# Kernel tuning notes

Hardware: AMD Instinct MI355X
Metric: run time of the kernel (lower is better)

Reference implementation:

```python
import jax, jax.numpy as jnp
import numpy as np


def rmsnorm(x, w):
    eps = jnp.finfo(x.dtype).eps  # torch nn.RMSNorm default eps=None -> finfo eps
    return x * jax.lax.rsqrt(jnp.mean(x * x, axis=-1, keepdims=True) + eps) * w


def rotary_freqs(n, d, dtype):
    inv_freq = 1.0 / (10000.0 ** (np.arange(0, d, 2, dtype=np.float32) / d))
    t = np.arange(n, dtype=np.float32)
    f = np.einsum('i,j->ij', t, inv_freq)
    f = np.concatenate([f, f], axis=-1)  # (n, d)
    return jnp.asarray(f, dtype=dtype)


def rotate_half(x):
    x1, x2 = jnp.split(x, 2, axis=-1)
    return jnp.concatenate([-x2, x1], axis=-1)


def local_window_attention(q, k, v, w):
    # q,k,v: (b,h,n,d); causal sliding window, exact window: key j allowed iff 0 <= i-j <= w
    b, h, n, d = q.shape
    nw = n // w
    scale = d ** -0.5
    qw = (q * scale).reshape(b, h, nw, w, d)
    kw = k.reshape(b, h, nw, w, d)
    vw = v.reshape(b, h, nw, w, d)
    shift_prev = lambda t: jnp.concatenate([jnp.zeros_like(t[:, :, :1]), t[:, :, :-1]], axis=2)
    kcat = jnp.concatenate([shift_prev(kw), kw], axis=3)  # (b,h,nw,2w,d)
    vcat = jnp.concatenate([shift_prev(vw), vw], axis=3)
    sim = jnp.einsum('bhnid,bhnjd->bhnij', qw, kcat)  # (b,h,nw,w,2w)
    i_pos = jnp.arange(w)[:, None]
    j_rel = jnp.arange(2 * w)[None, :] - w  # relative key position within window pair
    rel = i_pos - j_rel
    allowed = (rel >= 0) & (rel <= w)  # causal + exact window size
    win_idx = jnp.arange(nw)[:, None, None]
    abs_j_ok = (win_idx * w + j_rel[None]) >= 0  # mask zero-padded keys of first window
    mask = allowed[None] & abs_j_ok  # (nw, w, 2w)
    neg = -jnp.finfo(sim.dtype).max
    sim = jnp.where(mask[None, None], sim, neg)
    attn = jax.nn.softmax(sim, axis=-1)
    out = jnp.einsum('bhnij,bhnjd->bhnid', attn, vcat)
    return out.reshape(b, h, n, d)


def setup_inputs() -> dict:
    key = jax.random.key(0)
    k1, k2, k3 = jax.random.split(key, 3)
    b, n, dim, heads, dim_head, window = 4, 8192, 1024, 16, 64, 64
    dim_inner = heads * dim_head
    x = jax.random.normal(k1, (b, n, dim), dtype=jnp.float32)
    w_norm = jnp.ones((dim,), dtype=jnp.float32)
    w_qkv = jax.random.normal(k2, (dim, 3 * dim_inner), dtype=jnp.float32) * 0.02
    w_o = jax.random.normal(k3, (dim_inner, dim), dtype=jnp.float32) * 0.02
    return {"x": x, "w_norm": w_norm, "w_qkv": w_qkv, "w_o": w_o, "heads": heads, "window_size": window}


def reference(x, w_norm, w_qkv, w_o, heads, window_size):
    b, n, dim = x.shape
    xn = rmsnorm(x, w_norm)
    qkv = xn @ w_qkv  # (b,n,3*h*d)
    q, k, v = jnp.split(qkv, 3, axis=-1)
    split = lambda t: t.reshape(b, n, heads, -1).transpose(0, 2, 1, 3)  # b h n d
    q, k, v = split(q), split(k), split(v)
    d = q.shape[-1]
    freqs = rotary_freqs(n, d, q.dtype)  # (n,d)
    cos, sin = jnp.cos(freqs), jnp.sin(freqs)
    rope = lambda t: t * cos + rotate_half(t) * sin
    q, k = rope(q), rope(k)
    out = local_window_attention(q, k, v, window_size)
    out = out.transpose(0, 2, 1, 3).reshape(b, n, -1)  # merge heads
    return out @ w_o
```

## Files before the change

### kernel.cpp

```cpp
#include <hip/hip_runtime.h>
#include <stdint.h>
#include <math.h>

typedef __attribute__((ext_vector_type(4))) float  f32x4;
typedef __attribute__((ext_vector_type(8))) short  bf16x8;
typedef __attribute__((ext_vector_type(4))) short  s16x4;

#define AS1 __attribute__((address_space(1)))
#define AS3 __attribute__((address_space(3)))

static __device__ __forceinline__ void async_ld16(void* lds, const void* g) {
  __builtin_amdgcn_global_load_lds((const AS1 uint32_t*)g, (AS3 uint32_t*)lds, 16, 0, 0);
}

static __device__ __forceinline__ float bf2f(short u) {
  union { uint32_t i; float f; } v; v.i = ((uint32_t)(uint16_t)u) << 16; return v.f;
}
static __device__ __forceinline__ short f2bf(float f) {
  union { float f; uint32_t i; } v; v.f = f;
  uint32_t x = v.i;
  return (short)((x + 0x7fffu + ((x >> 16) & 1u)) >> 16);
}

__global__ __launch_bounds__(256) void k_trig(float* __restrict__ ct, float* __restrict__ st) {
  int idx = blockIdx.x * 256 + threadIdx.x;
  int pos = idx >> 5, i = idx & 31;
  double invf = 1.0 / pow(10000.0, (double)(2 * i) / 64.0);
  float f = (float)((double)pos * invf);
  ct[idx] = cosf(f);
  st[idx] = sinf(f);
}

__global__ __launch_bounds__(256) void k_transpose_cvt(const float* __restrict__ in,
                                                       short* __restrict__ out, int K, int N) {
  __shared__ float tile[64][65];
  int n0 = blockIdx.x * 64, k0 = blockIdx.y * 64;
  int tid = threadIdx.x;
  #pragma unroll
  for (int it = 0; it < 16; ++it) {
    int idx = tid + it * 256;
    int r = idx >> 6, c = idx & 63;
    tile[r][c] = in[(size_t)(k0 + r) * N + (n0 + c)];
  }
  __syncthreads();
  #pragma unroll
  for (int it = 0; it < 16; ++it) {
    int idx = tid + it * 256;
    int r = idx >> 6, c = idx & 63;
    out[(size_t)(n0 + r) * K + (k0 + c)] = f2bf(tile[c][r]);
  }
}

__global__ __launch_bounds__(256) void k_rmsnorm(const float* __restrict__ x,
                                                 const float* __restrict__ w,
                                                 short* __restrict__ xn) {
  int row = blockIdx.x;
  const float* xr = x + (size_t)row * 1024;
  int tid = threadIdx.x;
  f32x4 v = *(const f32x4*)(xr + (tid << 2));
  float ss = v[0]*v[0] + v[1]*v[1] + v[2]*v[2] + v[3]*v[3];
  #pragma unroll
  for (int off = 1; off < 64; off <<= 1) ss += __shfl_xor(ss, off);
  __shared__ float red[4];
  if ((tid & 63) == 0) red[tid >> 6] = ss;
  __syncthreads();
  float tot = red[0] + red[1] + red[2] + red[3];
  float inv = rsqrtf(tot * (1.0f / 1024.0f) + 1.1920928955078125e-07f);
  f32x4 wv = *(const f32x4*)(w + (tid << 2));
  s16x4 o;
  #pragma unroll
  for (int e = 0; e < 4; ++e) o[e] = f2bf(v[e] * inv * wv[e]);
  *(s16x4*)(xn + (size_t)row * 1024 + (tid << 2)) = o;
}

template<bool OUT_BF16>
__global__ __launch_bounds__(256) void k_gemm(const short* __restrict__ A,
                                              const short* __restrict__ Bt,
                                              void* __restrict__ Cout,
                                              int M, int N, int K) {
  __shared__ short As[128 * 32];
  __shared__ short Bs[128 * 32];
  const int tid = threadIdx.x;
  const int wave = tid >> 6, lane = tid & 63;
  const int g = lane >> 4, r = lane & 15;

  const int nwg = gridDim.x, bid = blockIdx.x;
  const int cpx = nwg >> 3;
  const int swz = (bid & 7) * cpx + (bid >> 3);
  const int nbx = N >> 7;
  const int bx = swz % nbx, by = swz / nbx;
  const int m0 = by << 7, n0 = bx << 7;
  const int wr = wave >> 1, wc = wave & 1;

  f32x4 acc[4][4];
  #pragma unroll
  for (int i = 0; i < 4; ++i)
    #pragma unroll
    for (int j = 0; j < 4; ++j)
      #pragma unroll
      for (int e = 0; e < 4; ++e) acc[i][j][e] = 0.0f;

  const int ci0 = wave * 128 + lane, ci1 = ci0 + 64;
  const int ar0 = ci0 >> 2, as0 = (ci0 & 3) ^ ((ar0 >> 1) & 3);
  const int ar1 = ci1 >> 2, as1 = (ci1 & 3) ^ ((ar1 >> 1) & 3);
  const short* Ag0 = A  + (size_t)(m0 + ar0) * K + as0 * 8;
  const short* Ag1 = A  + (size_t)(m0 + ar1) * K + as1 * 8;
  const short* Bg0 = Bt + (size_t)(n0 + ar0) * K + as0 * 8;
  const short* Bg1 = Bt + (size_t)(n0 + ar1) * K + as1 * 8;
  short* Al0 = &As[(wave * 128 + 0)  * 8];
  short* Al1 = &As[(wave * 128 + 64) * 8];
  short* Bl0 = &Bs[(wave * 128 + 0)  * 8];
  short* Bl1 = &Bs[(wave * 128 + 64) * 8];

  for (int k0 = 0; k0 < K; k0 += 32) {
    async_ld16(Al0, Ag0 + k0);
    async_ld16(Al1, Ag1 + k0);
    async_ld16(Bl0, Bg0 + k0);
    async_ld16(Bl1, Bg1 + k0);
    __syncthreads();
    bf16x8 af[4], bfr[4];
    #pragma unroll
    for (int m = 0; m < 4; ++m) {
      int row = wr * 64 + m * 16 + r;
      af[m] = *(const bf16x8*)&As[row * 32 + ((g ^ ((row >> 1) & 3)) * 8)];
    }
    #pragma unroll
    for (int n = 0; n < 4; ++n) {
      int row = wc * 64 + n * 16 + r;
      bfr[n] = *(const bf16x8*)&Bs[row * 32 + ((g ^ ((row >> 1) & 3)) * 8)];
    }
    #pragma unroll
    for (int m = 0; m < 4; ++m)
      #pragma unroll
      for (int n = 0; n < 4; ++n)
        acc[m][n] = __builtin_amdgcn_mfma_f32_16x16x32_bf16(af[m], bfr[n], acc[m][n], 0, 0, 0);
    __syncthreads();
  }

  if (OUT_BF16) {
    short* C = (short*)Cout;
    #pragma unroll
    for (int m = 0; m < 4; ++m) {
      int rowb = m0 + wr * 64 + m * 16 + g * 4;
      #pragma unroll
      for (int n = 0; n < 4; ++n) {
        int col = n0 + wc * 64 + n * 16 + r;
        #pragma unroll
        for (int q = 0; q < 4; ++q) C[(size_t)(rowb + q) * N + col] = f2bf(acc[m][n][q]);
      }
    }
  } else {
    float* C = (float*)Cout;
    #pragma unroll
    for (int m = 0; m < 4; ++m) {
      int rowb = m0 + wr * 64 + m * 16 + g * 4;
      #pragma unroll
      for (int n = 0; n < 4; ++n) {
        int col = n0 + wc * 64 + n * 16 + r;
        #pragma unroll
        for (int q = 0; q < 4; ++q) C[(size_t)(rowb + q) * N + col] = acc[m][n][q];
      }
    }
  }
}

__global__ __launch_bounds__(256) void k_rope(short* __restrict__ qkv,
                                              const float* __restrict__ ct,
                                              const float* __restrict__ st) {
  int t = blockIdx.x * 256 + threadIdx.x;
  int row = t >> 7, rem = t & 127;
  int hp = rem >> 2, d0 = (rem & 3) * 8;
  int part = hp >> 4, h = hp & 15;
  size_t base = (size_t)row * 3072 + part * 1024 + h * 64;
  int pos = row & 8191;
  bf16x8 lo = *(const bf16x8*)(qkv + base + d0);
  bf16x8 hi = *(const bf16x8*)(qkv + base + d0 + 32);
  f32x4 c0 = *(const f32x4*)(ct + pos * 32 + d0);
  f32x4 c1 = *(const f32x4*)(ct + pos * 32 + d0 + 4);
  f32x4 s0 = *(const f32x4*)(st + pos * 32 + d0);
  f32x4 s1 = *(const f32x4*)(st + pos * 32 + d0 + 4);
  bf16x8 olo, ohi;
  #pragma unroll
  for (int e = 0; e < 8; ++e) {
    float c = (e < 4) ? c0[e & 3] : c1[e & 3];
    float s = (e < 4) ? s0[e & 3] : s1[e & 3];
    float xl = bf2f(lo[e]), xh = bf2f(hi[e]);
    olo[e] = f2bf(xl * c - xh * s);
    ohi[e] = f2bf(xh * c + xl * s);
  }
  *(bf16x8*)(qkv + base + d0) = olo;
  *(bf16x8*)(qkv + base + d0 + 32) = ohi;
}

__global__ __launch_bounds__(256) void k_attn(const short* __restrict__ qkv,
                                              short* __restrict__ aout) {
  const int win = blockIdx.x, h = blockIdx.y, bb = blockIdx.z;
  __shared__ short Qs[64 * 64];
  __shared__ short Ks[128 * 64];
  __shared__ short Vt[64 * 128];
  __shared__ short Ps[64 * 128];

  const int tid = threadIdx.x;
  const int wave = tid >> 6, lane = tid & 63;
  const int g = lane >> 4, r = lane & 15;
  const size_t bbase = (size_t)bb * 8192;

  #pragma unroll
  for (int t = 0; t < 2; ++t) {
    int i = wave * 128 + t * 64 + lane;
    int row = i >> 3, seg = i & 7;
    int sseg = seg ^ (row & 7);
    const short* gp = qkv + (bbase + win * 64 + row) * 3072 + h * 64 + sseg * 8;
    async_ld16(&Qs[(wave * 128 + t * 64) * 8], gp);
  }
  #pragma unroll
  for (int t = 0; t < 4; ++t) {
    int i = wave * 256 + t * 64 + lane;
    int row = i >> 3, seg = i & 7;
    int sseg = seg ^ (row & 7);
    int kpos = win * 64 - 64 + row; if (kpos < 0) kpos = 0;
    const short* gp = qkv + (bbase + kpos) * 3072 + 1024 + h * 64 + sseg * 8;
    async_ld16(&Ks[(wave * 256 + t * 64) * 8], gp);
  }
  #pragma unroll
  for (int t = 0; t < 4; ++t) {
    int task = tid + t * 256;
    int j = task >> 3, dseg = task & 7;
    int kpos = win * 64 - 64 + j; if (kpos < 0) kpos = 0;
    bf16x8 v = *(const bf16x8*)(qkv + (bbase + kpos) * 3072 + 2048 + h * 64 + dseg * 8);
    #pragma unroll
    for (int e = 0; e < 8; ++e) {
      int d = dseg * 8 + e;
      Vt[d * 128 + (((j >> 3) ^ (d & 15)) * 8) + (j & 7)] = v[e];
    }
  }
  __syncthreads();

  f32x4 sac[8];
  #pragma unroll
  for (int n = 0; n < 8; ++n)
    #pragma unroll
    for (int e = 0; e < 4; ++e) sac[n][e] = 0.0f;
  {
    bf16x8 aq[2];
    #pragma unroll
    for (int ks = 0; ks < 2; ++ks) {
      int row = wave * 16 + r;
      aq[ks] = *(const bf16x8*)&Qs[row * 64 + (((ks * 4 + g) ^ (row & 7)) * 8)];
    }
    #pragma unroll
    for (int n = 0; n < 8; ++n)
      #pragma unroll
      for (int ks = 0; ks < 2; ++ks) {
        int key = n * 16 + r;
        bf16x8 bk = *(const bf16x8*)&Ks[key * 64 + (((ks * 4 + g) ^ (key & 7)) * 8)];
        sac[n] = __builtin_amdgcn_mfma_f32_16x16x32_bf16(aq[ks], bk, sac[n], 0, 0, 0);
      }
  }

  float pm[8][4], mx[4], sm[4];
  #pragma unroll
  for (int q = 0; q < 4; ++q) mx[q] = -3.0e38f;
  #pragma unroll
  for (int n = 0; n < 8; ++n)
    #pragma unroll
    for (int q = 0; q < 4; ++q) {
      int iq = wave * 16 + g * 4 + q;
      int j = n * 16 + r;
      bool ok = (j >= iq) && (j <= iq + 64) && (win > 0 || j >= 64);
      float s = ok ? sac[n][q] * 0.125f : -3.0e38f;
      pm[n][q] = s;
      mx[q] = fmaxf(mx[q], s);
    }
  #pragma unroll
  for (int q = 0; q < 4; ++q)
    #pragma unroll
    for (int off = 1; off < 16; off <<= 1) mx[q] = fmaxf(mx[q], __shfl_xor(mx[q], off));
  #pragma unroll
  for (int q = 0; q < 4; ++q) sm[q] = 0.0f;
  #pragma unroll
  for (int n = 0; n < 8; ++n)
    #pragma unroll
    for (int q = 0; q < 4; ++q) {
      float p = __expf(pm[n][q] - mx[q]);
      pm[n][q] = p;
      sm[q] += p;
    }
  #pragma unroll
  for (int q = 0; q < 4; ++q) {
    #pragma unroll
    for (int off = 1; off < 16; off <<= 1) sm[q] += __shfl_xor(sm[q], off);
    sm[q] = 1.0f / sm[q];
  }
  #pragma unroll
  for (int n = 0; n < 8; ++n)
    #pragma unroll
    for (int q = 0; q < 4; ++q) {
      int iq = wave * 16 + g * 4 + q;
      int j = n * 16 + r;
      Ps[iq * 128 + (((j >> 3) ^ (iq & 15)) * 8) + (j & 7)] = f2bf(pm[n][q] * sm[q]);
    }
  __syncthreads();

  f32x4 oac[4];
  #pragma unroll
  for (int n = 0; n < 4; ++n)
    #pragma unroll
    for (int e = 0; e < 4; ++e) oac[n][e] = 0.0f;
  #pragma unroll
  for (int ks = 0; ks < 4; ++ks) {
    int rowp = wave * 16 + r;
    bf16x8 ap = *(const bf16x8*)&Ps[rowp * 128 + (((ks * 4 + g) ^ (rowp & 15)) * 8)];
    #pragma unroll
    for (int n = 0; n < 4; ++n) {
      int d = n * 16 + r;
      bf16x8 bv = *(const bf16x8*)&Vt[d * 128 + (((ks * 4 + g) ^ (d & 15)) * 8)];
      oac[n] = __builtin_amdgcn_mfma_f32_16x16x32_bf16(ap, bv, oac[n], 0, 0, 0);
    }
  }
  #pragma unroll
  for (int n = 0; n < 4; ++n)
    #pragma unroll
    for (int q = 0; q < 4; ++q) {
      int iq = wave * 16 + g * 4 + q;
      int d = n * 16 + r;
      int pos = win * 64 + iq;
      aout[(bbase + pos) * 1024 + h * 64 + d] = f2bf(oac[n][q]);
    }
}

extern "C" void kernel_launch(void* const* d_in, const int* in_sizes, int n_in,
                              void* d_out, int out_size, void* d_ws, size_t ws_size,
                              hipStream_t stream) {
  const float* x      = (const float*)d_in[0];
  const float* w_norm = (const float*)d_in[1];
  const float* w_qkv  = (const float*)d_in[2];
  const float* w_o    = (const float*)d_in[3];
  float* out = (float*)d_out;
  (void)in_sizes; (void)n_in; (void)out_size; (void)ws_size;

  const int R = 4 * 8192;

  char* ws = (char*)d_ws;
  size_t off = 0;
  auto alloc = [&](size_t bytes) { char* p = ws + off; off += (bytes + 255) & ~(size_t)255; return p; };
  short* xn   = (short*)alloc((size_t)R * 1024 * 2);
  short* wqT  = (short*)alloc((size_t)3072 * 1024 * 2);
  short* woT  = (short*)alloc((size_t)1024 * 1024 * 2);
  short* qkv  = (short*)alloc((size_t)R * 3072 * 2);
  short* aout = (short*)alloc((size_t)R * 1024 * 2);
  float* ct   = (float*)alloc((size_t)8192 * 32 * 4);
  float* st   = (float*)alloc((size_t)8192 * 32 * 4);

  k_trig<<<1024, 256, 0, stream>>>(ct, st);
  k_transpose_cvt<<<dim3(3072 / 64, 1024 / 64), 256, 0, stream>>>(w_qkv, wqT, 1024, 3072);
  k_transpose_cvt<<<dim3(1024 / 64, 1024 / 64), 256, 0, stream>>>(w_o, woT, 1024, 1024);
  k_rmsnorm<<<R, 256, 0, stream>>>(x, w_norm, xn);
  k_gemm<true><<<(R / 128) * (3072 / 128), 256, 0, stream>>>(xn, wqT, qkv, R, 3072, 1024);
  k_rope<<<16384, 256, 0, stream>>>(qkv, ct, st);
  k_attn<<<dim3(128, 16, 4), 256, 0, stream>>>(qkv, aout);
  k_gemm<false><<<(R / 128) * (1024 / 128), 256, 0, stream>>>(aout, woT, out, R, 1024, 1024);
}
```

Before: 759.3 us.

## Replace GEMMs with 256x256 double-buffered pipelined kernel and fuse RoPE into epilogue

Replaces the 128x128 single-buffered GEMM with a 256x256-tile, 512-thread kernel. It double-buffers 64-wide K slices in LDS, interleaves async global-to-LDS loads with quarter-tile MFMA phases under explicit barriers and waitcnts, and raises wave priority around the MFMA blocks. The rotary embedding is applied to the fp32 accumulators in the QKV GEMM epilogue for the Q and K columns, which removes the separate rope pass over the qkv buffer. The larger tile uses 128KB of LDS and more registers per block, and fewer workgroups are launched for the smaller output GEMM.

```diff
diff --git a/kernel.cpp b/kernel.cpp
--- a/kernel.cpp
+++ b/kernel.cpp
@@ -21,6 +21,12 @@
   uint32_t x = v.i;
   return (short)((x + 0x7fffu + ((x >> 16) & 1u)) >> 16);
 }
+
+#define BAR()   __builtin_amdgcn_s_barrier()
+#define LGKM0() do { asm volatile("s_waitcnt lgkmcnt(0)" ::: "memory"); \
+                     __builtin_amdgcn_sched_barrier(0); } while (0)
+#define VMW4()  asm volatile("s_waitcnt vmcnt(4)" ::: "memory")
+#define PRIO(p) __builtin_amdgcn_s_setprio(p)
 
 __global__ __launch_bounds__(256) void k_trig(float* __restrict__ ct, float* __restrict__ st) {
   int idx = blockIdx.x * 256 + threadIdx.x;
@@ -73,123 +79,163 @@
   *(s16x4*)(xn + (size_t)row * 1024 + (tid << 2)) = o;
 }
 
-template<bool OUT_BF16>
-__global__ __launch_bounds__(256) void k_gemm(const short* __restrict__ A,
-                                              const short* __restrict__ Bt,
-                                              void* __restrict__ Cout,
-                                              int M, int N, int K) {
-  __shared__ short As[128 * 32];
-  __shared__ short Bs[128 * 32];
-  const int tid = threadIdx.x;
+#define STAGE(mi, P, rb, h, kt, buf) do {                                          \
+    const int lrb = (h) * 128 + wrow;                                              \
+    const short* _s0 = (P) + (size_t)((rb) + lrb + srow) * K + (kt) * 64 + xseg * 8;      \
+    const short* _s1 = (P) + (size_t)((rb) + lrb + 8 + srow) * K + (kt) * 64 + xseg * 8;  \
+    async_ld16(&lds[buf][mi][lrb * 64], _s0);                                      \
+    async_ld16(&lds[buf][mi][(lrb + 8) * 64], _s1);                                \
+  } while (0)
+
+#define RDA(buf, mh, m, kk) \
+  (*(const bf16x8*)&lds[buf][0][(wr * 128 + (mh) * 64 + (m) * 16 + r) * 64 + ((((kk) * 4 + g) ^ rs) * 8)])
+#define RDB(buf, nh, n, kk) \
+  (*(const bf16x8*)&lds[buf][1][(wc * 64 + (nh) * 32 + (n) * 16 + r) * 64 + ((((kk) * 4 + g) ^ rs) * 8)])
+
+template<bool OUT_BF16, bool ROPE>
+__global__ __launch_bounds__(512, 2) void k_gemm2(const short* __restrict__ A,
+                                                  const short* __restrict__ Bt,
+                                                  void* __restrict__ Cout,
+                                                  const float* __restrict__ ct,
+                                                  const float* __restrict__ st,
+                                                  int M, int N, int K) {
+  __shared__ short lds[2][2][256 * 64];
+  (void)M;
+  const int tid  = threadIdx.x;
   const int wave = tid >> 6, lane = tid & 63;
   const int g = lane >> 4, r = lane & 15;
+  const int wr = wave >> 2, wc = wave & 3;
+  const int rs = r & 7;
 
   const int nwg = gridDim.x, bid = blockIdx.x;
   const int cpx = nwg >> 3;
   const int swz = (bid & 7) * cpx + (bid >> 3);
-  const int nbx = N >> 7;
+  const int nbx = N >> 8;
   const int bx = swz % nbx, by = swz / nbx;
-  const int m0 = by << 7, n0 = bx << 7;
-  const int wr = wave >> 1, wc = wave & 1;
-
-  f32x4 acc[4][4];
-  #pragma unroll
-  for (int i = 0; i < 4; ++i)
+  const int m0 = by << 8, n0 = bx << 8;
+  const int NT = K >> 6;
+
+  const int srow = lane >> 3;
+  const int xseg = (lane & 7) ^ srow;
+  const int wrow = wave * 16;
+
+  f32x4 acc[8][4];
+  #pragma unroll
+  for (int i = 0; i < 8; ++i)
     #pragma unroll
     for (int j = 0; j < 4; ++j)
-      #pragma unroll
-      for (int e = 0; e < 4; ++e) acc[i][j][e] = 0.0f;
-
-  const int ci0 = wave * 128 + lane, ci1 = ci0 + 64;
-  const int ar0 = ci0 >> 2, as0 = (ci0 & 3) ^ ((ar0 >> 1) & 3);
-  const int ar1 = ci1 >> 2, as1 = (ci1 & 3) ^ ((ar1 >> 1) & 3);
-  const short* Ag0 = A  + (size_t)(m0 + ar0) * K + as0 * 8;
-  const short* Ag1 = A  + (size_t)(m0 + ar1) * K + as1 * 8;
-  const short* Bg0 = Bt + (size_t)(n0 + ar0) * K + as0 * 8;
-  const short* Bg1 = Bt + (size_t)(n0 + ar1) * K + as1 * 8;
-  short* Al0 = &As[(wave * 128 + 0)  * 8];
-  short* Al1 = &As[(wave * 128 + 64) * 8];
-  short* Bl0 = &Bs[(wave * 128 + 0)  * 8];
-  short* Bl1 = &Bs[(wave * 128 + 64) * 8];
-
-  for (int k0 = 0; k0 < K; k0 += 32) {
-    async_ld16(Al0, Ag0 + k0);
-    async_ld16(Al1, Ag1 + k0);
-    async_ld16(Bl0, Bg0 + k0);
-    async_ld16(Bl1, Bg1 + k0);
-    __syncthreads();
-    bf16x8 af[4], bfr[4];
-    #pragma unroll
-    for (int m = 0; m < 4; ++m) {
-      int row = wr * 64 + m * 16 + r;
-      af[m] = *(const bf16x8*)&As[row * 32 + ((g ^ ((row >> 1) & 3)) * 8)];
-    }
-    #pragma unroll
-    for (int n = 0; n < 4; ++n) {
-      int row = wc * 64 + n * 16 + r;
-      bfr[n] = *(const bf16x8*)&Bs[row * 32 + ((g ^ ((row >> 1) & 3)) * 8)];
-    }
+      acc[i][j] = (f32x4){0.f, 0.f, 0.f, 0.f};
+
+  STAGE(0, A,  m0, 0, 0, 0);
+  STAGE(0, A,  m0, 1, 0, 0);
+  STAGE(1, Bt, n0, 0, 0, 0);
+  STAGE(1, Bt, n0, 1, 0, 0);
+  STAGE(1, Bt, n0, 0, 1, 1);
+  STAGE(0, A,  m0, 0, 1, 1);
+  VMW4(); BAR();
+
+  bf16x8 a[4][2], b0[2][2], b1[2][2];
+  for (int t = 0; t < NT; ++t) {
+    const int cur = t & 1, nxt = cur ^ 1;
+    const int t1 = (t + 1 < NT) ? t + 1 : 0;
+    const int t2 = (t + 2 < NT) ? t + 2 : t + 2 - NT;
+
+    #pragma unroll
+    for (int m = 0; m < 4; ++m) { a[m][0] = RDA(cur, 0, m, 0); a[m][1] = RDA(cur, 0, m, 1); }
+    #pragma unroll
+    for (int n = 0; n < 2; ++n) { b0[n][0] = RDB(cur, 0, n, 0); b0[n][1] = RDB(cur, 0, n, 1); }
+    STAGE(0, A, m0, 1, t1, nxt);
+    BAR(); LGKM0(); PRIO(1);
     #pragma unroll
     for (int m = 0; m < 4; ++m)
       #pragma unroll
-      for (int n = 0; n < 4; ++n)
-        acc[m][n] = __builtin_amdgcn_mfma_f32_16x16x32_bf16(af[m], bfr[n], acc[m][n], 0, 0, 0);
-    __syncthreads();
+      for (int n = 0; n < 2; ++n)
+        #pragma unroll
+        for (int kk = 0; kk < 2; ++kk)
+          acc[m][n] = __builtin_amdgcn_mfma_f32_16x16x32_bf16(a[m][kk], b0[n][kk], acc[m][n], 0, 0, 0);
+    PRIO(0); BAR();
+
+    #pragma unroll
+    for (int n = 0; n < 2; ++n) { b1[n][0] = RDB(cur, 1, n, 0); b1[n][1] = RDB(cur, 1, n, 1); }
+    STAGE(1, Bt, n0, 1, t1, nxt);
+    BAR(); LGKM0(); PRIO(1);
+    #pragma unroll
+    for (int m = 0; m < 4; ++m)
+      #pragma unroll
+      for (int n = 0; n < 2; ++n)
+        #pragma unroll
+        for (int kk = 0; kk < 2; ++kk)
+          acc[m][2 + n] = __builtin_amdgcn_mfma_f32_16x16x32_bf16(a[m][kk], b1[n][kk], acc[m][2 + n], 0, 0, 0);
+    PRIO(0); BAR();
+
+    #pragma unroll
+    for (int m = 0; m < 4; ++m) { a[m][0] = RDA(cur, 1, m, 0); a[m][1] = RDA(cur, 1, m, 1); }
+    STAGE(1, Bt, n0, 0, t2, cur);
+    BAR(); LGKM0(); PRIO(1);
+    #pragma unroll
+    for (int m = 0; m < 4; ++m)
+      #pragma unroll
+      for (int n = 0; n < 2; ++n)
+        #pragma unroll
+        for (int kk = 0; kk < 2; ++kk)
+          acc[4 + m][2 + n] = __builtin_amdgcn_mfma_f32_16x16x32_bf16(a[m][kk], b1[n][kk], acc[4 + m][2 + n], 0, 0, 0);
+    PRIO(0); BAR();
+
+    STAGE(0, A, m0, 0, t2, cur);
+    PRIO(1);
+    #pragma unroll
+    for (int m = 0; m < 4; ++m)
+      #pragma unroll
+      for (int n = 0; n < 2; ++n)
+        #pragma unroll
+        for (int kk = 0; kk < 2; ++kk)
+          acc[4 + m][n] = __builtin_amdgcn_mfma_f32_16x16x32_bf16(a[m][kk], b0[n][kk], acc[4 + m][n], 0, 0, 0);
+    PRIO(0);
+    VMW4(); BAR();
   }
 
   if (OUT_BF16) {
     short* C = (short*)Cout;
-    #pragma unroll
-    for (int m = 0; m < 4; ++m) {
-      int rowb = m0 + wr * 64 + m * 16 + g * 4;
-      #pragma unroll
-      for (int n = 0; n < 4; ++n) {
-        int col = n0 + wc * 64 + n * 16 + r;
-        #pragma unroll
-        for (int q = 0; q < 4; ++q) C[(size_t)(rowb + q) * N + col] = f2bf(acc[m][n][q]);
+    const bool doRope = ROPE && (n0 < 2048);
+    #pragma unroll
+    for (int mi = 0; mi < 8; ++mi) {
+      const int rowb = m0 + wr * 128 + mi * 16 + g * 4;
+      if (doRope) {
+        #pragma unroll
+        for (int q = 0; q < 4; ++q) {
+          const int pos = (rowb + q) & 8191;
+          #pragma unroll
+          for (int ni = 0; ni < 2; ++ni) {
+            const float c = ct[pos * 32 + ni * 16 + r];
+            const float s = st[pos * 32 + ni * 16 + r];
+            const float p0 = acc[mi][ni][q], p1 = acc[mi][ni + 2][q];
+            acc[mi][ni][q]     = p0 * c - p1 * s;
+            acc[mi][ni + 2][q] = p1 * c + p0 * s;
+          }
+        }
+      }
+      #pragma unroll
+      for (int ni = 0; ni < 4; ++ni) {
+        const int col = n0 + wc * 64 + ni * 16 + r;
+        #pragma unroll
+        for (int q = 0; q < 4; ++q)
+          C[(size_t)(rowb + q) * N + col] = f2bf(acc[mi][ni][q]);
       }
     }
   } else {
     float* C = (float*)Cout;
     #pragma unroll
-    for (int m = 0; m < 4; ++m) {
-      int rowb = m0 + wr * 64 + m * 16 + g * 4;
-      #pragma unroll
-      for (int n = 0; n < 4; ++n) {
-        int col = n0 + wc * 64 + n * 16 + r;
-        #pragma unroll
-        for (int q = 0; q < 4; ++q) C[(size_t)(rowb + q) * N + col] = acc[m][n][q];
+    for (int mi = 0; mi < 8; ++mi) {
+      const int rowb = m0 + wr * 128 + mi * 16 + g * 4;
+      #pragma unroll
+      for (int ni = 0; ni < 4; ++ni) {
+        const int col = n0 + wc * 64 + ni * 16 + r;
+        #pragma unroll
+        for (int q = 0; q < 4; ++q)
+          C[(size_t)(rowb + q) * N + col] = acc[mi][ni][q];
       }
     }
   }
-}
-
-__global__ __launch_bounds__(256) void k_rope(short* __restrict__ qkv,
-                                              const float* __restrict__ ct,
-                                              const float* __restrict__ st) {
-  int t = blockIdx.x * 256 + threadIdx.x;
-  int row = t >> 7, rem = t & 127;
-  int hp = rem >> 2, d0 = (rem & 3) * 8;
-  int part = hp >> 4, h = hp & 15;
-  size_t base = (size_t)row * 3072 + part * 1024 + h * 64;
-  int pos = row & 8191;
-  bf16x8 lo = *(const bf16x8*)(qkv + base + d0);
-  bf16x8 hi = *(const bf16x8*)(qkv + base + d0 + 32);
-  f32x4 c0 = *(const f32x4*)(ct + pos * 32 + d0);
-  f32x4 c1 = *(const f32x4*)(ct + pos * 32 + d0 + 4);
-  f32x4 s0 = *(const f32x4*)(st + pos * 32 + d0);
-  f32x4 s1 = *(const f32x4*)(st + pos * 32 + d0 + 4);
-  bf16x8 olo, ohi;
-  #pragma unroll
-  for (int e = 0; e < 8; ++e) {
-    float c = (e < 4) ? c0[e & 3] : c1[e & 3];
-    float s = (e < 4) ? s0[e & 3] : s1[e & 3];
-    float xl = bf2f(lo[e]), xh = bf2f(hi[e]);
-    olo[e] = f2bf(xl * c - xh * s);
-    ohi[e] = f2bf(xh * c + xl * s);
-  }
-  *(bf16x8*)(qkv + base + d0) = olo;
-  *(bf16x8*)(qkv + base + d0 + 32) = ohi;
 }
 
 __global__ __launch_bounds__(256) void k_attn(const short* __restrict__ qkv,
@@ -356,8 +402,7 @@
   k_transpose_cvt<<<dim3(3072 / 64, 1024 / 64), 256, 0, stream>>>(w_qkv, wqT, 1024, 3072);
   k_transpose_cvt<<<dim3(1024 / 64, 1024 / 64), 256, 0, stream>>>(w_o, woT, 1024, 1024);
   k_rmsnorm<<<R, 256, 0, stream>>>(x, w_norm, xn);
-  k_gemm<true><<<(R / 128) * (3072 / 128), 256, 0, stream>>>(xn, wqT, qkv, R, 3072, 1024);
-  k_rope<<<16384, 256, 0, stream>>>(qkv, ct, st);
+  k_gemm2<true, true><<<(R / 256) * (3072 / 256), 512, 0, stream>>>(xn, wqT, qkv, ct, st, R, 3072, 1024);
   k_attn<<<dim3(128, 16, 4), 256, 0, stream>>>(qkv, aout);
-  k_gemm<false><<<(R / 128) * (1024 / 128), 256, 0, stream>>>(aout, woT, out, R, 1024, 1024);
-}
+  k_gemm2<false, false><<<(R / 256) * (1024 / 256), 512, 0, stream>>>(aout, woT, out, ct, st, R, 1024, 1024);
+}
```

After: 608.2 us. 19.9% less time.
